# Performance work log

Measured on AMD Instinct MI355X. Metric: run time of the kernel, lower is better.

Reference implementation:

```python
import jax, jax.numpy as jnp
import numpy as np

D_MODEL = 128
NUM_CLASSES = 32
ETA = 4.0
RC = 6.0
NR = 4          # ceil(D_MODEL / NUM_CLASSES)
# lmax = floor(sqrt(NR-1)) = 1 -> spherical harmonics l=0 and l=1 (4 components)


def setup_inputs() -> dict:
    key = jax.random.key(0)
    k1, k2 = jax.random.split(key)
    B, N = 256, 1024
    xyz = jax.random.normal(k1, (B, N, 3), dtype=jnp.float32) * 2.0
    cls = jax.random.randint(k2, (B, N), 0, NUM_CLASSES).astype(jnp.float32)
    x = jnp.concatenate([xyz, cls[..., None]], axis=-1)  # [B,N,4]
    return {"x": x}


def _forward(x):
    Rs = jnp.arange(NR, dtype=x.dtype) * (RC / NR)       # [NR] = [0,1.5,3,4.5]
    xyz = x[..., :3]
    r = jnp.sqrt(jnp.sum(xyz * xyz, axis=-1))            # [B,N]

    # radial basis: exp(-eta*(Rs - r)^2)                  -> [B,N,NR]
    radial = jnp.exp(-ETA * (Rs - r[..., None]) ** 2)

    # cosine cutoff (r clamped to Rc -> weight 0 beyond)  -> [B,N,1]
    rc = jnp.minimum(r, RC)
    env = (0.5 * jnp.cos(jnp.pi * rc / RC) + 0.5)[..., None]

    # real spherical harmonics l<=1 on unit directions, orthonormal norm,
    # m ordering (-l..l): [Y00, Y1,-1~y, Y1,0~z, Y1,1~x]  -> [B,N,NR]
    u = xyz / jnp.where(r > 0, r, 1.0)[..., None]
    y00 = 0.5 / jnp.sqrt(jnp.pi)
    c1 = jnp.sqrt(3.0 / (4.0 * jnp.pi))
    sh = jnp.stack(
        [jnp.full(r.shape, y00, dtype=x.dtype),
         c1 * u[..., 1], c1 * u[..., 2], c1 * u[..., 0]], axis=-1)

    prod = sh * radial * env                             # [B,N,NR]

    # per-class masked scatter: pos[b,n,:,c] = prod[b,n,:] where class==c and r!=0
    cls = x[..., 3].astype(jnp.int32)
    onehot = jax.nn.one_hot(cls, NUM_CLASSES, dtype=prod.dtype) * (r != 0)[..., None]
    pos = prod[..., :, None] * onehot[..., None, :]      # [B,N,NR,C]
    B, N = x.shape[0], x.shape[1]
    pos = pos.reshape(B, N, NR * NUM_CLASSES)[..., :D_MODEL]

    pos = jnp.nan_to_num(pos, nan=0.0)

    # torch F.normalize default dim=1 (neighbor axis), eps=1e-12
    norm = jnp.sqrt(jnp.sum(pos * pos, axis=1, keepdims=True))
    pos = pos / jnp.maximum(norm, 1e-12)

    # standardize along feature axis (torch std is unbiased, ddof=1)
    mean = jnp.mean(pos, axis=-1, keepdims=True)
    std = jnp.std(pos, axis=-1, ddof=1, keepdims=True)
    return (pos - mean) / (std + 1e-6)


def reference(x):
    return _forward(x)
```

## Files before the change

### kernel.cpp

```cpp
#include <hip/hip_runtime.h>
#include <math.h>

#define B_SZ 256
#define N_SZ 1024
#define D_MODEL 128
#define NUM_CLASSES 32

#define K_EXP (-5.770780163555854f)
#define K_COS (1.0f / 12.0f)

__device__ __forceinline__ void compute_prod(const float4 xv, float& r, int& c, float p[4]) {
    const float y00 = 0.28209479177387814f;
    const float c1  = 0.48860251190291992f;
    float r2 = xv.x * xv.x + xv.y * xv.y + xv.z * xv.z;
    r = sqrtf(r2);
    c = (int)xv.w;
    float inv_r = (r > 0.0f) ? __builtin_amdgcn_rcpf(r) : 0.0f;
    float ux = xv.x * inv_r, uy = xv.y * inv_r, uz = xv.z * inv_r;
    float rc = fminf(r, 6.0f);
    float env = 0.5f * __builtin_amdgcn_cosf(rc * K_COS) + 0.5f;
    float d0 = 0.0f - r, d1 = 1.5f - r, d2 = 3.0f - r, d3 = 4.5f - r;
    float rad0 = __builtin_amdgcn_exp2f(d0 * d0 * K_EXP);
    float rad1 = __builtin_amdgcn_exp2f(d1 * d1 * K_EXP);
    float rad2 = __builtin_amdgcn_exp2f(d2 * d2 * K_EXP);
    float rad3 = __builtin_amdgcn_exp2f(d3 * d3 * K_EXP);
    p[0] = y00 * rad0 * env;
    p[1] = c1 * uy * rad1 * env;
    p[2] = c1 * uz * rad2 * env;
    p[3] = c1 * ux * rad3 * env;
}

__global__ __launch_bounds__(1024) void ape_fused_kernel(const float* __restrict__ x,
                                                         float* __restrict__ out) {
    __shared__ float nsq[D_MODEL];
    __shared__ float invn[D_MODEL];
    __shared__ float sp0[N_SZ], sp1[N_SZ], sp2[N_SZ], sp3[N_SZ];
    __shared__ int   scls[N_SZ];

    const int b = blockIdx.x;
    const int t = threadIdx.x;
    if (t < D_MODEL) nsq[t] = 0.0f;
    __syncthreads();

    {
        float4 xv = ((const float4*)x)[(size_t)b * N_SZ + t];
        float r; int c; float p[4];
        compute_prod(xv, r, c, p);
        if (r <= 0.0f) { p[0] = p[1] = p[2] = p[3] = 0.0f; }
        sp0[t] = p[0]; sp1[t] = p[1]; sp2[t] = p[2]; sp3[t] = p[3];
        scls[t] = c;
        if (r > 0.0f) {
            atomicAdd(&nsq[0 * NUM_CLASSES + c], p[0] * p[0]);
            atomicAdd(&nsq[1 * NUM_CLASSES + c], p[1] * p[1]);
            atomicAdd(&nsq[2 * NUM_CLASSES + c], p[2] * p[2]);
            atomicAdd(&nsq[3 * NUM_CLASSES + c], p[3] * p[3]);
        }
    }
    __syncthreads();

    if (t < D_MODEL) {
        invn[t] = __builtin_amdgcn_rcpf(fmaxf(sqrtf(nsq[t]), 1e-12f));
    }
    __syncthreads();

    const int sub = t & 3;
    const int hb = sub * 4;
#pragma unroll
    for (int k = 0; k < 4; ++k) {
        const int n = k * 256 + (t >> 2);
        const int c = scls[n];
        float pn0 = sp0[n] * invn[0 * NUM_CLASSES + c];
        float pn1 = sp1[n] * invn[1 * NUM_CLASSES + c];
        float pn2 = sp2[n] * invn[2 * NUM_CLASSES + c];
        float pn3 = sp3[n] * invn[3 * NUM_CLASSES + c];
        float sum = pn0 + pn1 + pn2 + pn3;
        float mean = sum * (1.0f / 128.0f);
        float sumsq = pn0 * pn0 + pn1 * pn1 + pn2 * pn2 + pn3 * pn3;
        float var = fmaxf((sumsq - 128.0f * mean * mean) * (1.0f / 127.0f), 0.0f);
        float inv_std = __builtin_amdgcn_rcpf(sqrtf(var) + 1e-6f);
        float bneg = -mean * inv_std;
        float amb[4];
        amb[0] = pn0 * inv_std + bneg;
        amb[1] = pn1 * inv_std + bneg;
        amb[2] = pn2 * inv_std + bneg;
        amb[3] = pn3 * inv_std + bneg;

        float4* ob = (float4*)out + ((size_t)b * N_SZ + n) * 32 + sub;
#pragma unroll
        for (int j = 0; j < 8; ++j) {
            const float a = amb[j >> 1];
            const int cb = (j & 1) * 16 + hb;
            float4 o;
            o.x = (cb + 0 == c) ? a : bneg;
            o.y = (cb + 1 == c) ? a : bneg;
            o.z = (cb + 2 == c) ? a : bneg;
            o.w = (cb + 3 == c) ? a : bneg;
            ob[j * 4] = o;
        }
    }
}

extern "C" void kernel_launch(void* const* d_in, const int* in_sizes, int n_in,
                              void* d_out, int out_size, void* d_ws, size_t ws_size,
                              hipStream_t stream) {
    const float* x = (const float*)d_in[0];
    float* out = (float*)d_out;
    ape_fused_kernel<<<B_SZ, 1024, 0, stream>>>(x, out);
}
```

Measured before the change: 138.6 us.

## Split fused kernel into prep pass and wide output-writing kernel

Separates per-point normalization and standardization into a prep kernel that stores compact per-point records in workspace. A second kernel with many small blocks expands those records into the full output. This targets the poor occupancy of one 1024-thread block per batch during the write-bound phase. In exchange it adds a second launch and an extra round trip of intermediate data through global memory.

```diff
diff --git a/kernel.cpp b/kernel.cpp
--- a/kernel.cpp
+++ b/kernel.cpp
@@ -30,73 +30,73 @@
     p[3] = c1 * ux * rad3 * env;
 }
 
-__global__ __launch_bounds__(1024) void ape_fused_kernel(const float* __restrict__ x,
-                                                         float* __restrict__ out) {
+__global__ __launch_bounds__(1024) void ape_prep_kernel(const float* __restrict__ x,
+                                                        float4* __restrict__ recA,
+                                                        float2* __restrict__ recB) {
     __shared__ float nsq[D_MODEL];
     __shared__ float invn[D_MODEL];
-    __shared__ float sp0[N_SZ], sp1[N_SZ], sp2[N_SZ], sp3[N_SZ];
-    __shared__ int   scls[N_SZ];
-
     const int b = blockIdx.x;
     const int t = threadIdx.x;
     if (t < D_MODEL) nsq[t] = 0.0f;
     __syncthreads();
 
-    {
-        float4 xv = ((const float4*)x)[(size_t)b * N_SZ + t];
-        float r; int c; float p[4];
-        compute_prod(xv, r, c, p);
-        if (r <= 0.0f) { p[0] = p[1] = p[2] = p[3] = 0.0f; }
-        sp0[t] = p[0]; sp1[t] = p[1]; sp2[t] = p[2]; sp3[t] = p[3];
-        scls[t] = c;
-        if (r > 0.0f) {
-            atomicAdd(&nsq[0 * NUM_CLASSES + c], p[0] * p[0]);
-            atomicAdd(&nsq[1 * NUM_CLASSES + c], p[1] * p[1]);
-            atomicAdd(&nsq[2 * NUM_CLASSES + c], p[2] * p[2]);
-            atomicAdd(&nsq[3 * NUM_CLASSES + c], p[3] * p[3]);
-        }
+    float4 xv = ((const float4*)x)[(size_t)b * N_SZ + t];
+    float r; int c; float p[4];
+    compute_prod(xv, r, c, p);
+    if (r <= 0.0f) { p[0] = p[1] = p[2] = p[3] = 0.0f; }
+    if (r > 0.0f) {
+        atomicAdd(&nsq[0 * NUM_CLASSES + c], p[0] * p[0]);
+        atomicAdd(&nsq[1 * NUM_CLASSES + c], p[1] * p[1]);
+        atomicAdd(&nsq[2 * NUM_CLASSES + c], p[2] * p[2]);
+        atomicAdd(&nsq[3 * NUM_CLASSES + c], p[3] * p[3]);
     }
     __syncthreads();
-
     if (t < D_MODEL) {
         invn[t] = __builtin_amdgcn_rcpf(fmaxf(sqrtf(nsq[t]), 1e-12f));
     }
     __syncthreads();
 
-    const int sub = t & 3;
+    float pn0 = p[0] * invn[0 * NUM_CLASSES + c];
+    float pn1 = p[1] * invn[1 * NUM_CLASSES + c];
+    float pn2 = p[2] * invn[2 * NUM_CLASSES + c];
+    float pn3 = p[3] * invn[3 * NUM_CLASSES + c];
+    float sum = pn0 + pn1 + pn2 + pn3;
+    float mean = sum * (1.0f / 128.0f);
+    float sumsq = pn0 * pn0 + pn1 * pn1 + pn2 * pn2 + pn3 * pn3;
+    float var = fmaxf((sumsq - 128.0f * mean * mean) * (1.0f / 127.0f), 0.0f);
+    float inv_std = __builtin_amdgcn_rcpf(sqrtf(var) + 1e-6f);
+    float bneg = -mean * inv_std;
+    const size_t pt = (size_t)b * N_SZ + t;
+    recA[pt] = make_float4(pn0 * inv_std + bneg, pn1 * inv_std + bneg,
+                           pn2 * inv_std + bneg, pn3 * inv_std + bneg);
+    recB[pt] = make_float2(bneg, __int_as_float(c));
+}
+
+__global__ __launch_bounds__(256) void ape_write_kernel(const float4* __restrict__ recA,
+                                                        const float2* __restrict__ recB,
+                                                        float* __restrict__ out) {
+    const int gid = blockIdx.x * 256 + threadIdx.x;
+    const int pt = gid >> 2;
+    const int sub = gid & 3;
+
+    const float4 amb4 = recA[pt];
+    const float2 bb = recB[pt];
+    const float bneg = bb.x;
+    const int c = __float_as_int(bb.y);
+    const float amb[4] = {amb4.x, amb4.y, amb4.z, amb4.w};
+
+    float4* ob = (float4*)out + (size_t)pt * 32 + sub;
     const int hb = sub * 4;
 #pragma unroll
-    for (int k = 0; k < 4; ++k) {
-        const int n = k * 256 + (t >> 2);
-        const int c = scls[n];
-        float pn0 = sp0[n] * invn[0 * NUM_CLASSES + c];
-        float pn1 = sp1[n] * invn[1 * NUM_CLASSES + c];
-        float pn2 = sp2[n] * invn[2 * NUM_CLASSES + c];
-        float pn3 = sp3[n] * invn[3 * NUM_CLASSES + c];
-        float sum = pn0 + pn1 + pn2 + pn3;
-        float mean = sum * (1.0f / 128.0f);
-        float sumsq = pn0 * pn0 + pn1 * pn1 + pn2 * pn2 + pn3 * pn3;
-        float var = fmaxf((sumsq - 128.0f * mean * mean) * (1.0f / 127.0f), 0.0f);
-        float inv_std = __builtin_amdgcn_rcpf(sqrtf(var) + 1e-6f);
-        float bneg = -mean * inv_std;
-        float amb[4];
-        amb[0] = pn0 * inv_std + bneg;
-        amb[1] = pn1 * inv_std + bneg;
-        amb[2] = pn2 * inv_std + bneg;
-        amb[3] = pn3 * inv_std + bneg;
-
-        float4* ob = (float4*)out + ((size_t)b * N_SZ + n) * 32 + sub;
-#pragma unroll
-        for (int j = 0; j < 8; ++j) {
-            const float a = amb[j >> 1];
-            const int cb = (j & 1) * 16 + hb;
-            float4 o;
-            o.x = (cb + 0 == c) ? a : bneg;
-            o.y = (cb + 1 == c) ? a : bneg;
-            o.z = (cb + 2 == c) ? a : bneg;
-            o.w = (cb + 3 == c) ? a : bneg;
-            ob[j * 4] = o;
-        }
+    for (int j = 0; j < 8; ++j) {
+        const float a = amb[j >> 1];
+        const int cb = (j & 1) * 16 + hb;
+        float4 o;
+        o.x = (cb + 0 == c) ? a : bneg;
+        o.y = (cb + 1 == c) ? a : bneg;
+        o.z = (cb + 2 == c) ? a : bneg;
+        o.w = (cb + 3 == c) ? a : bneg;
+        ob[j * 4] = o;
     }
 }
 
@@ -105,5 +105,11 @@
                               hipStream_t stream) {
     const float* x = (const float*)d_in[0];
     float* out = (float*)d_out;
-    ape_fused_kernel<<<B_SZ, 1024, 0, stream>>>(x, out);
+    float4* recA = (float4*)d_ws;
+    float2* recB = (float2*)((char*)d_ws + (size_t)B_SZ * N_SZ * sizeof(float4));
+
+    ape_prep_kernel<<<B_SZ, 1024, 0, stream>>>(x, recA, recB);
+
+    const int total_threads = B_SZ * N_SZ * 4;
+    ape_write_kernel<<<total_threads / 256, 256, 0, stream>>>(recA, recB, out);
 }
```

New measurement: 142.3 us. +2.7%, slower.
